# Performance work log

Measured on AMD Instinct MI355X. Metric: run time of the kernel, lower is better.

## Reference

```python
import jax, jax.numpy as jnp
import numpy as np

B, S, D, E, TOP_K = 16, 2048, 240, 8, 2


def setup_inputs() -> dict:
    key = jax.random.key(0)
    k1, k2, k3 = jax.random.split(key, 3)
    scale = 1.0 / np.sqrt(D)
    return {
        "x": jax.random.normal(k1, (B, S, D), dtype=jnp.float32),
        "gate_w": jax.random.normal(k2, (E, D), dtype=jnp.float32) * scale,
        "gate_b": jnp.zeros((E,), dtype=jnp.float32),
        "expert_w": jax.random.normal(k3, (E, D, D), dtype=jnp.float32) * scale,
        "expert_b": jnp.zeros((E, D), dtype=jnp.float32),
    }


def reference(x, gate_w, gate_b, expert_w, expert_b):
    # Gating: softmax over experts, pick top-k, renormalize.
    logits = jnp.einsum("bsd,ed->bse", x, gate_w) + gate_b          # [B,S,E]
    gate_weights = jax.nn.softmax(logits, axis=-1)
    topk_w, topk_i = jax.lax.top_k(gate_weights, TOP_K)             # [B,S,K]
    topk_w = topk_w / jnp.sum(topk_w, axis=-1, keepdims=True)
    # Scatter renormalized top-k weights back to dense per-expert weights.
    onehot = jax.nn.one_hot(topk_i, E, dtype=x.dtype)               # [B,S,K,E]
    w_full = jnp.sum(topk_w[..., None] * onehot, axis=-2)           # [B,S,E]
    # Expert linears (torch Linear: y = x @ W^T + b), combined by gate weight.
    h = jnp.einsum("bsd,eod->bseo", x, expert_w) + expert_b         # [B,S,E,D]
    return jnp.einsum("bseo,bse->bso", h, w_full)                   # [B,S,D]
```

## Files before the change

### kernel.cpp

```cpp
#include <hip/hip_runtime.h>
#include <hip/hip_bf16.h>

#define TOKENS 32768
#define Dm 240
#define DP 256
#define NE 8
#define BK 32
#define NCHUNK 8
#define TILE_M 64
#define NB 64
#define CSTR 16

typedef __bf16 bf16x8 __attribute__((ext_vector_type(8)));
typedef float  f32x4  __attribute__((ext_vector_type(4)));

__device__ __forceinline__ float b2f(unsigned short u) {
    union { unsigned int i; float f; } v; v.i = ((unsigned int)u) << 16; return v.f;
}
__device__ __forceinline__ float b2f_lo(unsigned u) {
    union { unsigned int i; float f; } v; v.i = u << 16; return v.f;
}
__device__ __forceinline__ float b2f_hi(unsigned u) {
    union { unsigned int i; float f; } v; v.i = u & 0xFFFF0000u; return v.f;
}
__device__ __forceinline__ unsigned short f2b(float f) {
    unsigned int i = __builtin_bit_cast(unsigned int, f);
    unsigned int r = (i + 0x7FFFu + ((i >> 16) & 1u)) >> 16;
    return (unsigned short)r;
}
__device__ __forceinline__ unsigned short f2h(float f) {
    _Float16 h = (_Float16)f;
    union { _Float16 h; unsigned short u; } v; v.h = h; return v.u;
}
__device__ __forceinline__ float h2f(unsigned short u) {
    union { _Float16 h; unsigned short u; } v; v.u = u; return (float)v.h;
}
__device__ __forceinline__ uint4 pack8(float4 a, float4 b) {
    union { unsigned short u[8]; uint4 v; } r;
    r.u[0] = f2b(a.x); r.u[1] = f2b(a.y); r.u[2] = f2b(a.z); r.u[3] = f2b(a.w);
    r.u[4] = f2b(b.x); r.u[5] = f2b(b.y); r.u[6] = f2b(b.z); r.u[7] = f2b(b.w);
    return r.v;
}

__device__ __forceinline__ void gload_lds16(const void* g, void* l) {
    __builtin_amdgcn_global_load_lds(
        (const __attribute__((address_space(1))) void*)g,
        (__attribute__((address_space(3))) void*)l,
        16, 0, 0);
}

__device__ __forceinline__ bool block_detect_f32(const unsigned short* x,
                                                 int tid, int* dh) {
    if (tid == 0) *dh = 0;
    __syncthreads();
    if (tid < 256) {
        uint4 q = *(const uint4*)&x[tid * 8];
        unsigned w[4] = {q.x, q.y, q.z, q.w};
        int hits = 0;
        #pragma unroll
        for (int i = 0; i < 4; i++) {
            if ((((w[i] & 0xFFFFu) >> 7) & 0xFFu) >= 0xC0u) hits++;
            if ((((w[i] >> 16)      >> 7) & 0xFFu) >= 0xC0u) hits++;
        }
        if (hits) atomicAdd(dh, hits);
    }
    __syncthreads();
    return *dh > 8;
}

__global__ __launch_bounds__(256) void wconv_kernel(
    const void* __restrict__ ewv, const void* __restrict__ ebv,
    const unsigned short* __restrict__ xus,
    int* __restrict__ flag, int* __restrict__ cnt,
    unsigned short* __restrict__ wpad, float* __restrict__ ebpad)
{
    __shared__ int dh;
    int tid = threadIdx.x;
    const bool f32 = block_detect_f32(xus, tid, &dh);
    if (blockIdx.x == 0) {
        if (tid == 0) flag[0] = f32 ? 1 : 0;
        for (int i = tid; i < NB * CSTR; i += 256) cnt[i] = 0;
    }

    int gidx = blockIdx.x * 256 + tid;

    if (gidx < NE * DP) {
        int e = gidx >> 8, n = gidx & 255;
        float bv = 0.f;
        if (n < Dm)
            bv = f32 ? ((const float*)ebv)[e * Dm + n]
                     : b2f(((const unsigned short*)ebv)[e * Dm + n]);
        ebpad[gidx] = bv;
    }

    int n = gidx & 255;
    int s = (gidx >> 8) & 3;
    int c = (gidx >> 10) & 7;
    int e = gidx >> 13;
    int k = c * 32 + s * 8;
    uint4 v = make_uint4(0, 0, 0, 0);
    if (n < Dm && k < Dm) {
        if (f32) {
            const float* src = (const float*)ewv + ((long)e * Dm + n) * Dm + k;
            v = pack8(*(const float4*)src, *(const float4*)(src + 4));
        } else {
            v = *(const uint4*)((const unsigned short*)ewv + ((long)e * Dm + n) * Dm + k);
        }
    }
    *(uint4*)&wpad[(long)gidx * 8] = v;
}

__global__ __launch_bounds__(256) void gate_kernel(
    const void* __restrict__ xv, const void* __restrict__ gwv,
    const void* __restrict__ gbv,
    int* __restrict__ cnt, unsigned* __restrict__ rt,
    unsigned short* __restrict__ xpad)
{
    __shared__ float gwsF[NE * Dm];
    __shared__ int h[NB];
    __shared__ int base[NB];
    __shared__ int dh;

    int tid = threadIdx.x;
    if (tid < NB) h[tid] = 0;
    const bool f32 = block_detect_f32((const unsigned short*)xv, tid, &dh);

    if (f32) {
        if (tid < 240) {
            const float* s = (const float*)gwv + tid * 8;
            float4 a = *(const float4*)s;
            float4 b4 = *(const float4*)(s + 4);
            float* d = &gwsF[tid * 8];
            *(float4*)d = a; *(float4*)(d + 4) = b4;
        }
    } else {
        if (tid < 240) {
            unsigned short* gb16 = (unsigned short*)gwsF;
            *(uint4*)&gb16[tid * 8] =
                *(const uint4*)((const unsigned short*)gwv + tid * 8);
        }
    }
    __syncthreads();

    int grp = tid >> 3;
    int j   = tid & 7;
    int t   = blockIdx.x * 32 + grp;

    float acc[NE] = {0.f, 0.f, 0.f, 0.f, 0.f, 0.f, 0.f, 0.f};
    unsigned short* xo = xpad + (long)t * DP;

    if (f32) {
        const float* xf = (const float*)xv + (long)t * Dm;
        #pragma unroll
        for (int i = 0; i < 4; i++) {
            int g = j + 8 * i;
            if (g < 30) {
                float4 xa = *(const float4*)&xf[g * 8];
                float4 xb = *(const float4*)&xf[g * 8 + 4];
                *(uint4*)&xo[g * 8] = pack8(xa, xb);
                #pragma unroll
                for (int e = 0; e < NE; e++) {
                    const float* gp = &gwsF[e * Dm + g * 8];
                    float4 ga = *(const float4*)gp;
                    float4 gc = *(const float4*)(gp + 4);
                    acc[e] += xa.x * ga.x + xa.y * ga.y + xa.z * ga.z + xa.w * ga.w
                            + xb.x * gc.x + xb.y * gc.y + xb.z * gc.z + xb.w * gc.w;
                }
            } else {
                *(uint4*)&xo[g * 8] = make_uint4(0, 0, 0, 0);
            }
        }
    } else {
        const unsigned short* xb = (const unsigned short*)xv + (long)t * Dm;
        const unsigned short* gb16 = (const unsigned short*)gwsF;
        #pragma unroll
        for (int i = 0; i < 4; i++) {
            int g = j + 8 * i;
            if (g < 30) {
                uint4 xq = *(const uint4*)&xb[g * 8];
                *(uint4*)&xo[g * 8] = xq;
                float x0 = b2f_lo(xq.x), x1 = b2f_hi(xq.x);
                float x2 = b2f_lo(xq.y), x3 = b2f_hi(xq.y);
                float x4 = b2f_lo(xq.z), x5 = b2f_hi(xq.z);
                float x6 = b2f_lo(xq.w), x7 = b2f_hi(xq.w);
                #pragma unroll
                for (int e = 0; e < NE; e++) {
                    uint4 gq = *(const uint4*)&gb16[e * Dm + g * 8];
                    acc[e] += x0 * b2f_lo(gq.x) + x1 * b2f_hi(gq.x)
                            + x2 * b2f_lo(gq.y) + x3 * b2f_hi(gq.y)
                            + x4 * b2f_lo(gq.z) + x5 * b2f_hi(gq.z)
                            + x6 * b2f_lo(gq.w) + x7 * b2f_hi(gq.w);
                }
            } else {
                *(uint4*)&xo[g * 8] = make_uint4(0, 0, 0, 0);
            }
        }
    }

    #pragma unroll
    for (int m = 1; m < 8; m <<= 1)
        #pragma unroll
        for (int e = 0; e < NE; e++)
            acc[e] += __shfl_xor(acc[e], m, 64);

    int bb = 0; float w0 = 0.f;
    if (j == 0) {
        #pragma unroll
        for (int e = 0; e < NE; e++)
            acc[e] += f32 ? ((const float*)gbv)[e]
                          : b2f(((const unsigned short*)gbv)[e]);
        float l0 = -1e30f; int e0 = 0;
        #pragma unroll
        for (int e = 0; e < NE; e++) if (acc[e] > l0) { l0 = acc[e]; e0 = e; }
        float l1 = -1e30f; int e1 = 0;
        #pragma unroll
        for (int e = 0; e < NE; e++) if (e != e0 && acc[e] > l1) { l1 = acc[e]; e1 = e; }
        w0 = 1.f / (1.f + __expf(l1 - l0));
        bb = e0 * 8 + e1;
        atomicAdd(&h[bb], 1);
    }
    __syncthreads();
    if (tid < NB) {
        int i = (tid + blockIdx.x) & (NB - 1);
        int c = h[i];
        if (c) base[i] = atomicAdd(&cnt[i * CSTR], c);
        h[i] = 0;
    }
    __syncthreads();
    if (j == 0) {
        int o = atomicAdd(&h[bb], 1);
        rt[bb * TOKENS + base[bb] + o] = ((unsigned)t << 16) | (unsigned)f2h(w0);
    }
}

__global__ __launch_bounds__(512, 2) void expert_kernel(
    const unsigned short* __restrict__ xp,
    const unsigned short* __restrict__ wp,
    const float* __restrict__ ebpad,
    const int* __restrict__ flag,
    const int* __restrict__ cnt, const unsigned* __restrict__ rt,
    void* __restrict__ outv)
{
    __shared__ __align__(16) unsigned short Xc[NCHUNK][4][64][8];
    __shared__ int cntS[NB];

    const bool f32o = (*flag != 0);
    int tid = threadIdx.x;
    if (tid < NB) cntS[tid] = cnt[tid * CSTR];
    __syncthreads();

    int nwg = gridDim.x;
    int fid = blockIdx.x;
    if ((nwg & 7) == 0)
        fid = (blockIdx.x & 7) * (nwg >> 3) + (blockIdx.x >> 3);

    int b = -1, t = 0, accn = 0;
    for (int i = 0; i < NB; i++) {
        int ti = (cntS[i] + 63) >> 6;
        if (fid < accn + ti) { b = i; t = fid - accn; break; }
        accn += ti;
    }
    if (b < 0) return;
    int e0 = b >> 3, e1 = b & 7;
    int ne = cntS[b];
    int m0 = t * TILE_M;
    int rows = min(TILE_M, ne - m0);

    int lane = tid & 63;
    int w    = tid >> 6;

    unsigned rvp = rt[b * TOKENS + min(m0 + lane, ne - 1)];
    int   tokL = (int)(rvp >> 16);
    float w0L  = h2f((unsigned short)(rvp & 0xFFFFu));

    const unsigned short* xbase = xp + (long)tokL * DP;
    #pragma unroll
    for (int i = 0; i < 4; i++)
        gload_lds16(xbase + w * BK + i * 8, &Xc[w][i][0][0]);
    __syncthreads();

    int frow = lane & 15;
    int slot = lane >> 4;
    const unsigned short* wb0 = wp + (long)e0 * 65536 + slot * 2048
                                   + (w * 32 + frow) * 8;
    const unsigned short* wb1 = wp + (long)e1 * 65536 + slot * 2048
                                   + (w * 32 + frow) * 8;

    f32x4 acc0[4][2] = {};
    f32x4 acc1[4][2] = {};

    #pragma unroll
    for (int c = 0; c < NCHUNK; c++) {
        bf16x8 a[4], b0[2], b1[2];
        #pragma unroll
        for (int mt = 0; mt < 4; mt++)
            a[mt] = *(const bf16x8*)&Xc[c][slot][mt * 16 + frow][0];
        #pragma unroll
        for (int nt = 0; nt < 2; nt++) {
            b0[nt] = *(const bf16x8*)&wb0[c * 8192 + nt * 128];
            b1[nt] = *(const bf16x8*)&wb1[c * 8192 + nt * 128];
        }
        #pragma unroll
        for (int nt = 0; nt < 2; nt++)
            #pragma unroll
            for (int mt = 0; mt < 4; mt++) {
                acc0[mt][nt] = __builtin_amdgcn_mfma_f32_16x16x32_bf16(
                    a[mt], b0[nt], acc0[mt][nt], 0, 0, 0);
                acc1[mt][nt] = __builtin_amdgcn_mfma_f32_16x16x32_bf16(
                    a[mt], b1[nt], acc1[mt][nt], 0, 0, 0);
            }
    }

    int colg = lane & 15;
    int rq   = (lane >> 4) << 2;
    float b0n[2], b1n[2];
    #pragma unroll
    for (int nt = 0; nt < 2; nt++) {
        int n = w * 32 + nt * 16 + colg;
        b0n[nt] = ebpad[e0 * DP + n];
        b1n[nt] = ebpad[e1 * DP + n];
    }
    #pragma unroll
    for (int mt = 0; mt < 4; mt++) {
        #pragma unroll
        for (int r = 0; r < 4; r++) {
            int m = mt * 16 + rq + r;
            int   tok = __shfl(tokL, m);
            float w0  = __shfl(w0L, m);
            float w1  = 1.f - w0;
            if (m < rows) {
                #pragma unroll
                for (int nt = 0; nt < 2; nt++) {
                    int n = w * 32 + nt * 16 + colg;
                    if (n < Dm) {
                        float val = (acc0[mt][nt][r] + b0n[nt]) * w0
                                  + (acc1[mt][nt][r] + b1n[nt]) * w1;
                        long idx = (long)tok * Dm + n;
                        if (f32o) ((float*)outv)[idx] = val;
                        else      ((unsigned short*)outv)[idx] = f2b(val);
                    }
                }
            }
        }
    }
}

__global__ void detect_kernel(const unsigned short* __restrict__ x, int* flag,
                              int* __restrict__ cnt) {
    int lane = threadIdx.x;
    cnt[lane] = 0;
    int hits = 0;
    for (int i = lane; i < 2048; i += 64) {
        unsigned e = (x[i] >> 7) & 0xFFu;
        if (e >= 0xC0u) hits++;
    }
    #pragma unroll
    for (int off = 32; off >= 1; off >>= 1) hits += __shfl_xor(hits, off, 64);
    if (lane == 0) flag[0] = (hits > 8) ? 1 : 0;
}

__global__ void init_kernel(int* cnt) {
    if (threadIdx.x < 16) cnt[threadIdx.x] = 0;
}

__global__ void zero_kernel(void* outv, const int* flag, int nelem) {
    long i = (long)blockIdx.x * blockDim.x + threadIdx.x;
    long stride = (long)gridDim.x * blockDim.x;
    if (*flag) {
        float* o = (float*)outv;
        for (; i < nelem; i += stride) o[i] = 0.f;
    } else {
        unsigned* o = (unsigned*)outv;
        long n = nelem >> 1;
        for (; i < n; i += stride) o[i] = 0u;
    }
}

template<bool FP32>
__global__ __launch_bounds__(256) void gate_fb_kernel(
    const void* __restrict__ xv, const void* __restrict__ gwv,
    const void* __restrict__ gbv, const int* __restrict__ flag,
    int* __restrict__ cnt, unsigned* __restrict__ rt, int cap)
{
    if ((*flag != 0) != FP32) return;
    __shared__ unsigned rv[256];
    __shared__ int h[16];
    __shared__ int base[16];

    int tid = threadIdx.x;
    if (tid < 16) h[tid] = 0;
    int t = blockIdx.x * 256 + tid;

    float acc[NE];
    #pragma unroll
    for (int e = 0; e < NE; e++)
        acc[e] = FP32 ? ((const float*)gbv)[e]
                      : b2f(((const unsigned short*)gbv)[e]);

    if (FP32) {
        const float* xf  = (const float*)xv + (long)t * Dm;
        const float* gwf = (const float*)gwv;
        for (int k = 0; k < Dm; k += 8) {
            float4 xa = *(const float4*)&xf[k];
            float4 xb = *(const float4*)&xf[k + 4];
            #pragma unroll
            for (int e = 0; e < NE; e++) {
                float4 ga = *(const float4*)&gwf[e * Dm + k];
                float4 gb = *(const float4*)&gwf[e * Dm + k + 4];
                acc[e] += xa.x * ga.x + xa.y * ga.y + xa.z * ga.z + xa.w * ga.w
                        + xb.x * gb.x + xb.y * gb.y + xb.z * gb.z + xb.w * gb.w;
            }
        }
    } else {
        const unsigned short* xb  = (const unsigned short*)xv + (long)t * Dm;
        const unsigned short* gwb = (const unsigned short*)gwv;
        for (int k = 0; k < Dm; k += 8) {
            uint4 xq = *(const uint4*)&xb[k];
            float x0 = b2f_lo(xq.x), x1 = b2f_hi(xq.x);
            float x2 = b2f_lo(xq.y), x3 = b2f_hi(xq.y);
            float x4 = b2f_lo(xq.z), x5 = b2f_hi(xq.z);
            float x6 = b2f_lo(xq.w), x7 = b2f_hi(xq.w);
            #pragma unroll
            for (int e = 0; e < NE; e++) {
                uint4 gq = *(const uint4*)&gwb[e * Dm + k];
                acc[e] += x0 * b2f_lo(gq.x) + x1 * b2f_hi(gq.x)
                        + x2 * b2f_lo(gq.y) + x3 * b2f_hi(gq.y)
                        + x4 * b2f_lo(gq.z) + x5 * b2f_hi(gq.z)
                        + x6 * b2f_lo(gq.w) + x7 * b2f_hi(gq.w);
            }
        }
    }

    float l0 = -1e30f; int e0 = 0;
    #pragma unroll
    for (int e = 0; e < NE; e++) if (acc[e] > l0) { l0 = acc[e]; e0 = e; }
    float l1 = -1e30f; int e1 = 0;
    #pragma unroll
    for (int e = 0; e < NE; e++) if (e != e0 && acc[e] > l1) { l1 = acc[e]; e1 = e; }
    float w0 = 1.f / (1.f + __expf(l1 - l0));

    rv[tid] = ((unsigned)e1 << 20) | ((unsigned)e0 << 16) | (unsigned)f2h(w0);
    __syncthreads();

    {
        unsigned v = rv[tid];
        atomicAdd(&h[(v >> 16) & 7], 1);
        atomicAdd(&h[8 + ((v >> 20) & 7)], 1);
    }
    __syncthreads();

    if (tid < 16) {
        base[tid] = atomicAdd(&cnt[tid], h[tid]);
        h[tid] = 0;
    }
    __syncthreads();

    {
        unsigned v = rv[tid];
        int tt = blockIdx.x * 256 + tid;
        int a0 = (v >> 16) & 7;
        int a1 = (v >> 20) & 7;
        unsigned short hw0 = (unsigned short)(v & 0xFFFFu);
        int o0 = atomicAdd(&h[a0], 1);
        int p0 = base[a0] + o0;
        if (p0 < cap) rt[a0 * cap + p0] = ((unsigned)tt << 16) | hw0;
        int o1 = atomicAdd(&h[8 + a1], 1);
        int p1 = base[8 + a1] + o1;
        if (p1 < cap) rt[(8 + a1) * cap + p1] = ((unsigned)tt << 16) | (unsigned)f2h(1.f - h2f(hw0));
    }
}

template<bool FP32>
__global__ __launch_bounds__(256) void expert_fb_kernel(
    const void* __restrict__ xv, const void* __restrict__ ewv,
    const void* __restrict__ ebv, const int* __restrict__ flag,
    const int* __restrict__ cnt, const unsigned* __restrict__ rt, int cap,
    void* __restrict__ outv, int slotBase, int accumulate)
{
    if ((*flag != 0) != FP32) return;
    int e = blockIdx.y;
    int tile = blockIdx.x;
    int bucket = slotBase + e;
    int ne = min(cnt[bucket], cap);
    int m0 = tile * TILE_M;
    if (m0 >= ne) return;
    int rows = min(TILE_M, ne - m0);

    __shared__ __align__(16) unsigned short Wcf[2][256][40];
    __shared__ __align__(16) unsigned short Xcf[2][TILE_M][40];
    __shared__ int   tokS[TILE_M];
    __shared__ float twS[TILE_M];

    int tid = threadIdx.x;
    if (tid < TILE_M) {
        int i = min(m0 + tid, ne - 1);
        unsigned v = rt[bucket * cap + i];
        tokS[tid] = (int)(v >> 16);
        twS[tid]  = (tid < rows) ? h2f((unsigned short)(v & 0xFFFFu)) : 0.f;
    }
    __syncthreads();

    int srow = tid >> 2;
    int part = tid & 3;

    auto stage = [&](int c, int buf) {
        int kk = c * BK + part * 8;
        bool kvalid = (kk < Dm);
        if (FP32) {
            const float* xf = (const float*)xv;
            const float* Wf = (const float*)ewv + e * Dm * Dm;
            uint4 xq = make_uint4(0, 0, 0, 0);
            if (kvalid) {
                const float* s = &xf[(long)tokS[srow] * Dm + kk];
                xq = pack8(*(const float4*)s, *(const float4*)(s + 4));
            }
            *(uint4*)&Xcf[buf][srow][part * 8] = xq;
            #pragma unroll
            for (int it = 0; it < 4; it++) {
                int n = srow + it * 64;
                uint4 wq = make_uint4(0, 0, 0, 0);
                if (kvalid && n < Dm) {
                    const float* s = &Wf[(long)n * Dm + kk];
                    wq = pack8(*(const float4*)s, *(const float4*)(s + 4));
                }
                *(uint4*)&Wcf[buf][n][part * 8] = wq;
            }
        } else {
            const unsigned short* xb = (const unsigned short*)xv;
            const unsigned short* Wb = (const unsigned short*)ewv + e * Dm * Dm;
            uint4 xq = make_uint4(0, 0, 0, 0);
            if (kvalid) xq = *(const uint4*)&xb[(long)tokS[srow] * Dm + kk];
            *(uint4*)&Xcf[buf][srow][part * 8] = xq;
            #pragma unroll
            for (int it = 0; it < 4; it++) {
                int n = srow + it * 64;
                uint4 wq = make_uint4(0, 0, 0, 0);
                if (kvalid && n < Dm) wq = *(const uint4*)&Wb[(long)n * Dm + kk];
                *(uint4*)&Wcf[buf][n][part * 8] = wq;
            }
        }
    };

    int lane = tid & 63;
    int wv   = tid >> 6;
    int frow = lane & 15;
    int koff = (lane >> 4) * 8;

    f32x4 acc[TILE_M / 16][4] = {};

    stage(0, 0);
    __syncthreads();
    for (int c = 0; c < NCHUNK; c++) {
        int buf = c & 1;
        bf16x8 a[TILE_M / 16], b[4];
        #pragma unroll
        for (int mt = 0; mt < TILE_M / 16; mt++)
            a[mt] = *(const bf16x8*)&Xcf[buf][mt * 16 + frow][koff];
        #pragma unroll
        for (int nt = 0; nt < 4; nt++)
            b[nt] = *(const bf16x8*)&Wcf[buf][wv * 64 + nt * 16 + frow][koff];
        if (c + 1 < NCHUNK) stage(c + 1, (c + 1) & 1);
        #pragma unroll
        for (int mt = 0; mt < TILE_M / 16; mt++)
            #pragma unroll
            for (int nt = 0; nt < 4; nt++)
                acc[mt][nt] = __builtin_amdgcn_mfma_f32_16x16x32_bf16(
                    a[mt], b[nt], acc[mt][nt], 0, 0, 0);
        __syncthreads();
    }

    int colg  = lane & 15;
    int rquad = (lane >> 4) * 4;
    #pragma unroll
    for (int nt = 0; nt < 4; nt++) {
        int n = wv * 64 + nt * 16 + colg;
        if (n >= Dm) continue;
        float bnv = FP32 ? ((const float*)ebv)[e * Dm + n]
                         : b2f(((const unsigned short*)ebv)[e * Dm + n]);
        #pragma unroll
        for (int mt = 0; mt < TILE_M / 16; mt++) {
            #pragma unroll
            for (int r = 0; r < 4; r++) {
                int m = mt * 16 + rquad + r;
                if (m < rows) {
                    float val = (acc[mt][nt][r] + bnv) * twS[m];
                    long idx = (long)tokS[m] * Dm + n;
                    if (FP32) {
                        float* o = (float*)outv + idx;
                        *o = accumulate ? (*o + val) : val;
                    } else {
                        unsigned short* o = (unsigned short*)outv + idx;
                        *o = accumulate ? f2b(b2f(*o) + val) : f2b(val);
                    }
                }
            }
        }
    }
}

extern "C" void kernel_launch(void* const* d_in, const int* in_sizes, int n_in,
                              void* d_out, int out_size, void* d_ws, size_t ws_size,
                              hipStream_t stream) {
    const void* x  = d_in[0];
    const void* gw = d_in[1];
    const void* gb = d_in[2];
    const void* ew = d_in[3];
    const void* eb = d_in[4];

    char* ws = (char*)d_ws;
    int* flag = (int*)ws;
    int* cnt  = (int*)(ws + 64);

    const size_t EB_OFF = 64 + (size_t)NB * CSTR * 4;
    const size_t RT_OFF = EB_OFF + (size_t)NE * DP * 4;
    const size_t XP_OFF = RT_OFF + (size_t)NB * TOKENS * 4;
    const size_t WP_OFF = XP_OFF + (size_t)TOKENS * DP * 2;
    const size_t NEEDED = WP_OFF + (size_t)NE * NCHUNK * 8192 * 2;

    if (ws_size >= NEEDED) {
        float*          ebpad = (float*)(ws + EB_OFF);
        unsigned*       rt    = (unsigned*)(ws + RT_OFF);
        unsigned short* xpad  = (unsigned short*)(ws + XP_OFF);
        unsigned short* wpad  = (unsigned short*)(ws + WP_OFF);

        wconv_kernel<<<256, 256, 0, stream>>>(ew, eb, (const unsigned short*)x,
                                              flag, cnt, wpad, ebpad);
        gate_kernel<<<TOKENS / 32, 256, 0, stream>>>(x, gw, gb, cnt, rt, xpad);
        expert_kernel<<<TOKENS / TILE_M + NB, 512, 0, stream>>>(
            xpad, wpad, ebpad, flag, cnt, rt, d_out);
    } else {
        unsigned* rt = (unsigned*)(ws + 128);
        long capl = ((long)ws_size - 128) / (16 * sizeof(unsigned));
        if (capl > TOKENS) capl = TOKENS;
        if (capl < 64) capl = 64;
        int cap = (int)capl;
        int tiles = (cap + TILE_M - 1) / TILE_M;
        bool lossless = (cap >= TOKENS);
        int acc0 = lossless ? 0 : 1;

        detect_kernel<<<1, 64, 0, stream>>>((const unsigned short*)x, flag, cnt);
        init_kernel<<<1, 64, 0, stream>>>(cnt);
        gate_fb_kernel<false><<<TOKENS / 256, 256, 0, stream>>>(x, gw, gb, flag, cnt, rt, cap);
        gate_fb_kernel<true ><<<TOKENS / 256, 256, 0, stream>>>(x, gw, gb, flag, cnt, rt, cap);
        if (!lossless)
            zero_kernel<<<1024, 256, 0, stream>>>(d_out, flag, out_size);
        expert_fb_kernel<false><<<dim3(tiles, NE), 256, 0, stream>>>(x, ew, eb, flag, cnt, rt, cap, d_out, 0, acc0);
        expert_fb_kernel<true ><<<dim3(tiles, NE), 256, 0, stream>>>(x, ew, eb, flag, cnt, rt, cap, d_out, 0, acc0);
        expert_fb_kernel<false><<<dim3(tiles, NE), 256, 0, stream>>>(x, ew, eb, flag, cnt, rt, cap, d_out, 8, 1);
        expert_fb_kernel<true ><<<dim3(tiles, NE), 256, 0, stream>>>(x, ew, eb, flag, cnt, rt, cap, d_out, 8, 1);
    }
}
```

Measured before the change: 140.1 us.

## Fuse weight conversion into gate kernel and use 2D expert grid with tile loop

Weight and bias padding/conversion is merged into the gate kernel: the first 256 blocks convert weights and the remaining blocks do gating. The bucket counters are now zeroed with a memset instead of by the conversion kernel, which removes one kernel launch and one inter-kernel dependency. The expert kernel switches from a flattened prefix-sum tile lookup to a 2D grid (8 blocks per expert-pair bucket), where each block loops over that bucket's tiles with stride 8. This drops the per-block count scan, but a block may now run several tiles serially, and uneven bucket sizes can cause load imbalance.

After: 153.5 us. 9.6% more time.

```diff
diff --git a/kernel.cpp b/kernel.cpp
--- a/kernel.cpp
+++ b/kernel.cpp
@@ -68,53 +68,13 @@
     return *dh > 8;
 }
 
-__global__ __launch_bounds__(256) void wconv_kernel(
-    const void* __restrict__ ewv, const void* __restrict__ ebv,
-    const unsigned short* __restrict__ xus,
-    int* __restrict__ flag, int* __restrict__ cnt,
-    unsigned short* __restrict__ wpad, float* __restrict__ ebpad)
-{
-    __shared__ int dh;
-    int tid = threadIdx.x;
-    const bool f32 = block_detect_f32(xus, tid, &dh);
-    if (blockIdx.x == 0) {
-        if (tid == 0) flag[0] = f32 ? 1 : 0;
-        for (int i = tid; i < NB * CSTR; i += 256) cnt[i] = 0;
-    }
-
-    int gidx = blockIdx.x * 256 + tid;
-
-    if (gidx < NE * DP) {
-        int e = gidx >> 8, n = gidx & 255;
-        float bv = 0.f;
-        if (n < Dm)
-            bv = f32 ? ((const float*)ebv)[e * Dm + n]
-                     : b2f(((const unsigned short*)ebv)[e * Dm + n]);
-        ebpad[gidx] = bv;
-    }
-
-    int n = gidx & 255;
-    int s = (gidx >> 8) & 3;
-    int c = (gidx >> 10) & 7;
-    int e = gidx >> 13;
-    int k = c * 32 + s * 8;
-    uint4 v = make_uint4(0, 0, 0, 0);
-    if (n < Dm && k < Dm) {
-        if (f32) {
-            const float* src = (const float*)ewv + ((long)e * Dm + n) * Dm + k;
-            v = pack8(*(const float4*)src, *(const float4*)(src + 4));
-        } else {
-            v = *(const uint4*)((const unsigned short*)ewv + ((long)e * Dm + n) * Dm + k);
-        }
-    }
-    *(uint4*)&wpad[(long)gidx * 8] = v;
-}
-
-__global__ __launch_bounds__(256) void gate_kernel(
+__global__ __launch_bounds__(256) void gatewconv_kernel(
     const void* __restrict__ xv, const void* __restrict__ gwv,
     const void* __restrict__ gbv,
-    int* __restrict__ cnt, unsigned* __restrict__ rt,
-    unsigned short* __restrict__ xpad)
+    const void* __restrict__ ewv, const void* __restrict__ ebv,
+    int* __restrict__ flag, int* __restrict__ cnt,
+    unsigned* __restrict__ rt, unsigned short* __restrict__ xpad,
+    unsigned short* __restrict__ wpad, float* __restrict__ ebpad)
 {
     __shared__ float gwsF[NE * Dm];
     __shared__ int h[NB];
@@ -122,8 +82,42 @@
     __shared__ int dh;
 
     int tid = threadIdx.x;
+    const bool f32 = block_detect_f32((const unsigned short*)xv, tid, &dh);
+
+    if (blockIdx.x < 256) {
+        if (blockIdx.x == 0 && tid == 0) flag[0] = f32 ? 1 : 0;
+
+        int gidx = blockIdx.x * 256 + tid;
+
+        if (gidx < NE * DP) {
+            int e = gidx >> 8, n = gidx & 255;
+            float bv = 0.f;
+            if (n < Dm)
+                bv = f32 ? ((const float*)ebv)[e * Dm + n]
+                         : b2f(((const unsigned short*)ebv)[e * Dm + n]);
+            ebpad[gidx] = bv;
+        }
+
+        int n = gidx & 255;
+        int s = (gidx >> 8) & 3;
+        int c = (gidx >> 10) & 7;
+        int e = gidx >> 13;
+        int k = c * 32 + s * 8;
+        uint4 v = make_uint4(0, 0, 0, 0);
+        if (n < Dm && k < Dm) {
+            if (f32) {
+                const float* src = (const float*)ewv + ((long)e * Dm + n) * Dm + k;
+                v = pack8(*(const float4*)src, *(const float4*)(src + 4));
+            } else {
+                v = *(const uint4*)((const unsigned short*)ewv + ((long)e * Dm + n) * Dm + k);
+            }
+        }
+        *(uint4*)&wpad[(long)gidx * 8] = v;
+        return;
+    }
+
+    int gbid = blockIdx.x - 256;
     if (tid < NB) h[tid] = 0;
-    const bool f32 = block_detect_f32((const unsigned short*)xv, tid, &dh);
 
     if (f32) {
         if (tid < 240) {
@@ -144,7 +138,7 @@
 
     int grp = tid >> 3;
     int j   = tid & 7;
-    int t   = blockIdx.x * 32 + grp;
+    int t   = gbid * 32 + grp;
 
     float acc[NE] = {0.f, 0.f, 0.f, 0.f, 0.f, 0.f, 0.f, 0.f};
     unsigned short* xo = xpad + (long)t * DP;
@@ -221,7 +215,7 @@
     }
     __syncthreads();
     if (tid < NB) {
-        int i = (tid + blockIdx.x) & (NB - 1);
+        int i = (tid + gbid) & (NB - 1);
         int c = h[i];
         if (c) base[i] = atomicAdd(&cnt[i * CSTR], c);
         h[i] = 0;
@@ -242,42 +236,19 @@
     void* __restrict__ outv)
 {
     __shared__ __align__(16) unsigned short Xc[NCHUNK][4][64][8];
-    __shared__ int cntS[NB];
+
+    int b  = blockIdx.y;
+    int ne = cnt[b * CSTR];
+    if (ne == 0) return;
+    int ntile = (ne + 63) >> 6;
+    if ((int)blockIdx.x >= ntile) return;
 
     const bool f32o = (*flag != 0);
-    int tid = threadIdx.x;
-    if (tid < NB) cntS[tid] = cnt[tid * CSTR];
-    __syncthreads();
-
-    int nwg = gridDim.x;
-    int fid = blockIdx.x;
-    if ((nwg & 7) == 0)
-        fid = (blockIdx.x & 7) * (nwg >> 3) + (blockIdx.x >> 3);
-
-    int b = -1, t = 0, accn = 0;
-    for (int i = 0; i < NB; i++) {
-        int ti = (cntS[i] + 63) >> 6;
-        if (fid < accn + ti) { b = i; t = fid - accn; break; }
-        accn += ti;
-    }
-    if (b < 0) return;
     int e0 = b >> 3, e1 = b & 7;
-    int ne = cntS[b];
-    int m0 = t * TILE_M;
-    int rows = min(TILE_M, ne - m0);
-
+
+    int tid  = threadIdx.x;
     int lane = tid & 63;
     int w    = tid >> 6;
-
-    unsigned rvp = rt[b * TOKENS + min(m0 + lane, ne - 1)];
-    int   tokL = (int)(rvp >> 16);
-    float w0L  = h2f((unsigned short)(rvp & 0xFFFFu));
-
-    const unsigned short* xbase = xp + (long)tokL * DP;
-    #pragma unroll
-    for (int i = 0; i < 4; i++)
-        gload_lds16(xbase + w * BK + i * 8, &Xc[w][i][0][0]);
-    __syncthreads();
 
     int frow = lane & 15;
     int slot = lane >> 4;
@@ -285,32 +256,6 @@
                                    + (w * 32 + frow) * 8;
     const unsigned short* wb1 = wp + (long)e1 * 65536 + slot * 2048
                                    + (w * 32 + frow) * 8;
-
-    f32x4 acc0[4][2] = {};
-    f32x4 acc1[4][2] = {};
-
-    #pragma unroll
-    for (int c = 0; c < NCHUNK; c++) {
-        bf16x8 a[4], b0[2], b1[2];
-        #pragma unroll
-        for (int mt = 0; mt < 4; mt++)
-            a[mt] = *(const bf16x8*)&Xc[c][slot][mt * 16 + frow][0];
-        #pragma unroll
-        for (int nt = 0; nt < 2; nt++) {
-            b0[nt] = *(const bf16x8*)&wb0[c * 8192 + nt * 128];
-            b1[nt] = *(const bf16x8*)&wb1[c * 8192 + nt * 128];
-        }
-        #pragma unroll
-        for (int nt = 0; nt < 2; nt++)
-            #pragma unroll
-            for (int mt = 0; mt < 4; mt++) {
-                acc0[mt][nt] = __builtin_amdgcn_mfma_f32_16x16x32_bf16(
-                    a[mt], b0[nt], acc0[mt][nt], 0, 0, 0);
-                acc1[mt][nt] = __builtin_amdgcn_mfma_f32_16x16x32_bf16(
-                    a[mt], b1[nt], acc1[mt][nt], 0, 0, 0);
-            }
-    }
-
     int colg = lane & 15;
     int rq   = (lane >> 4) << 2;
     float b0n[2], b1n[2];
@@ -320,28 +265,71 @@
         b0n[nt] = ebpad[e0 * DP + n];
         b1n[nt] = ebpad[e1 * DP + n];
     }
-    #pragma unroll
-    for (int mt = 0; mt < 4; mt++) {
-        #pragma unroll
-        for (int r = 0; r < 4; r++) {
-            int m = mt * 16 + rq + r;
-            int   tok = __shfl(tokL, m);
-            float w0  = __shfl(w0L, m);
-            float w1  = 1.f - w0;
-            if (m < rows) {
+
+    for (int t = blockIdx.x; t < ntile; t += 8) {
+        int m0 = t * TILE_M;
+        int rows = min(TILE_M, ne - m0);
+
+        unsigned rvp = rt[b * TOKENS + min(m0 + lane, ne - 1)];
+        int   tokL = (int)(rvp >> 16);
+        float w0L  = h2f((unsigned short)(rvp & 0xFFFFu));
+
+        const unsigned short* xbase = xp + (long)tokL * DP;
+        #pragma unroll
+        for (int i = 0; i < 4; i++)
+            gload_lds16(xbase + w * BK + i * 8, &Xc[w][i][0][0]);
+        __syncthreads();
+
+        f32x4 acc0[4][2] = {};
+        f32x4 acc1[4][2] = {};
+
+        #pragma unroll
+        for (int c = 0; c < NCHUNK; c++) {
+            bf16x8 a[4], b0[2], b1[2];
+            #pragma unroll
+            for (int mt = 0; mt < 4; mt++)
+                a[mt] = *(const bf16x8*)&Xc[c][slot][mt * 16 + frow][0];
+            #pragma unroll
+            for (int nt = 0; nt < 2; nt++) {
+                b0[nt] = *(const bf16x8*)&wb0[c * 8192 + nt * 128];
+                b1[nt] = *(const bf16x8*)&wb1[c * 8192 + nt * 128];
+            }
+            #pragma unroll
+            for (int nt = 0; nt < 2; nt++)
                 #pragma unroll
-                for (int nt = 0; nt < 2; nt++) {
-                    int n = w * 32 + nt * 16 + colg;
-                    if (n < Dm) {
-                        float val = (acc0[mt][nt][r] + b0n[nt]) * w0
-                                  + (acc1[mt][nt][r] + b1n[nt]) * w1;
-                        long idx = (long)tok * Dm + n;
-                        if (f32o) ((float*)outv)[idx] = val;
-                        else      ((unsigned short*)outv)[idx] = f2b(val);
+                for (int mt = 0; mt < 4; mt++) {
+                    acc0[mt][nt] = __builtin_amdgcn_mfma_f32_16x16x32_bf16(
+                        a[mt], b0[nt], acc0[mt][nt], 0, 0, 0);
+                    acc1[mt][nt] = __builtin_amdgcn_mfma_f32_16x16x32_bf16(
+                        a[mt], b1[nt], acc1[mt][nt], 0, 0, 0);
+                }
+        }
+
+        #pragma unroll
+        for (int mt = 0; mt < 4; mt++) {
+            #pragma unroll
+            for (int r = 0; r < 4; r++) {
+                int m = mt * 16 + rq + r;
+                int   tok = __shfl(tokL, m);
+                float w0  = __shfl(w0L, m);
+                float w1  = 1.f - w0;
+                if (m < rows) {
+                    #pragma unroll
+                    for (int nt = 0; nt < 2; nt++) {
+                        int n = w * 32 + nt * 16 + colg;
+                        if (n < Dm) {
+                            float val = (acc0[mt][nt][r] + b0n[nt]) * w0
+                                      + (acc1[mt][nt][r] + b1n[nt]) * w1;
+                            long idx = (long)tok * Dm + n;
+                            if (f32o) ((float*)outv)[idx] = val;
+                            else      ((unsigned short*)outv)[idx] = f2b(val);
+                        }
                     }
                 }
             }
         }
+
+        if (t + 8 < ntile) __syncthreads();
     }
 }
 
@@ -623,10 +611,10 @@
         unsigned short* xpad  = (unsigned short*)(ws + XP_OFF);
         unsigned short* wpad  = (unsigned short*)(ws + WP_OFF);
 
-        wconv_kernel<<<256, 256, 0, stream>>>(ew, eb, (const unsigned short*)x,
-                                              flag, cnt, wpad, ebpad);
-        gate_kernel<<<TOKENS / 32, 256, 0, stream>>>(x, gw, gb, cnt, rt, xpad);
-        expert_kernel<<<TOKENS / TILE_M + NB, 512, 0, stream>>>(
+        hipMemsetAsync(ws, 0, EB_OFF, stream);
+        gatewconv_kernel<<<1280, 256, 0, stream>>>(
+            x, gw, gb, ew, eb, flag, cnt, rt, xpad, wpad, ebpad);
+        expert_kernel<<<dim3(8, NB), 512, 0, stream>>>(
             xpad, wpad, ebpad, flag, cnt, rt, d_out);
     } else {
         unsigned* rt = (unsigned*)(ws + 128);
```
